# Optimization experiments

Hardware: AMD Instinct MI355X
Metric: run time of the kernel (lower is better)

The kernel has to match this reference:

```python
import jax, jax.numpy as jnp
import numpy as np
import math

# module hyperparams (from init_kwargs)
H = 4          # num_heads
HID = 128      # hid_dim
DK = HID // H  # embed_time_k = 32
DIM = 64       # input_dim (value feature dim)
OUT = 128      # output_dim
NEG = -1e30


def setup_inputs() -> dict:
    key = jax.random.key(0)
    ks = jax.random.split(key, 10)
    B, SQ, SK = 16, 128, 256
    query = jax.random.normal(ks[0], (B, SQ, HID), jnp.float32)
    k_in = jax.random.normal(ks[1], (B, SK, HID), jnp.float32)
    value = jax.random.normal(ks[2], (B, SK, DIM), jnp.float32)
    mask = jax.random.randint(ks[3], (B, SK, DIM), 0, 2).astype(jnp.int32)
    s = 1.0 / math.sqrt(HID)
    Wq = jax.random.uniform(ks[4], (HID, HID), jnp.float32, -s, s)
    bq = jax.random.uniform(ks[5], (HID,), jnp.float32, -s, s)
    Wk = jax.random.uniform(ks[6], (HID, HID), jnp.float32, -s, s)
    bk = jax.random.uniform(ks[7], (HID,), jnp.float32, -s, s)
    so = 1.0 / math.sqrt(DIM * H)
    Wo = jax.random.uniform(ks[8], (OUT, DIM * H), jnp.float32, -so, so)
    bo = jax.random.uniform(ks[9], (OUT,), jnp.float32, -so, so)
    return {"query": query, "key": k_in, "value": value, "mask": mask,
            "Wq": Wq, "bq": bq, "Wk": Wk, "bk": bk, "Wo": Wo, "bo": bo}


def reference(query, key, value, mask, Wq, bq, Wk, bk, Wo, bo):
    B, SQ, _ = query.shape
    _, SK, D = value.shape
    # project and split heads: (B, S, HID) -> (B, H, S, DK)
    q = (query @ Wq.T + bq).reshape(B, SQ, H, DK).transpose(0, 2, 1, 3)
    k = (key @ Wk.T + bk).reshape(B, SK, H, DK).transpose(0, 2, 1, 3)
    # scores: (B, H, SQ, SK)
    scores = jnp.einsum('bhqd,bhkd->bhqk', q, k) / math.sqrt(DK)
    # per-channel mask: scores expand to (B, H, SQ, SK, D)
    m = (mask[:, None, None, :, :] != 0)  # (B,1,1,SK,D)
    scores5 = jnp.where(m, scores[..., None], NEG)
    # softmax over seq_k axis (axis=-2)
    p = jax.nn.softmax(scores5, axis=-2)
    # weighted sum over seq_k: (B, H, SQ, D)
    x = jnp.sum(p * value[:, None, None, :, :], axis=-2)
    # merge heads: (B, SQ, H*D) then output projection
    x = x.transpose(0, 2, 1, 3).reshape(B, SQ, H * D)
    return x @ Wo.T + bo
```

## Files before the change

kernel.cpp:

```cpp
#include <hip/hip_runtime.h>
#include <math.h>

#define B    16
#define SQn  128
#define SEQK 256
#define HID  128
#define NH   4
#define DK   32
#define DIM  64
#define OUTD 128

__global__ __launch_bounds__(256) void transpose3_kernel(
    const float* __restrict__ Wq, const float* __restrict__ Wk,
    const float* __restrict__ Wo,
    float* __restrict__ Wq_t, float* __restrict__ Wk_t, float* __restrict__ Wo_t)
{
    __shared__ float tile[16][17];
    const int z = blockIdx.z;
    const float* src; float* dst; int R, C;
    if (z == 0)      { src = Wq; dst = Wq_t; R = 128; C = 128; }
    else if (z == 1) { src = Wk; dst = Wk_t; R = 128; C = 128; }
    else             { src = Wo; dst = Wo_t; R = 128; C = 256; }
    const int c0 = blockIdx.x * 16, r0 = blockIdx.y * 16;
    if (c0 >= C) return;
    const int tx = threadIdx.x & 15, ty = threadIdx.x >> 4;
    tile[ty][tx] = src[(r0 + ty) * C + (c0 + tx)];
    __syncthreads();
    dst[(c0 + ty) * R + (r0 + tx)] = tile[tx][ty];
}

__global__ __launch_bounds__(256) void prep_kernel(
    const float* __restrict__ value, const int* __restrict__ mask,
    const float* __restrict__ bo, float* __restrict__ MVF, float* __restrict__ out)
{
    const int idx = blockIdx.x * 256 + threadIdx.x;
    const int NMV = B * SEQK * DIM;
    if (idx < NMV) {
        const int d = idx & 63, rest = idx >> 6;
        const float v = value[idx];
        const int   m = mask[idx];
        MVF[rest * 128 + d]      = m ? v : 0.f;
        MVF[rest * 128 + 64 + d] = m ? 1.f : 0.f;
    } else {
        const int o = idx - NMV;
        out[o] = bo[o & 127];
    }
}

__global__ __launch_bounds__(256) void projqk_kernel(
    const float* __restrict__ query, const float* __restrict__ key,
    const float* __restrict__ Wq_t, const float* __restrict__ Wk_t,
    const float* __restrict__ bq, const float* __restrict__ bk,
    float* __restrict__ qp, float* __restrict__ kp_t)
{
    __shared__ float in16[16 * 128];
    const int r0 = blockIdx.x * 16;
    const bool isQ = (r0 < 2048);
    const int t = threadIdx.x;

    const float4* src4 = (const float4*)(isQ ? (query + r0 * 128)
                                             : (key + (r0 - 2048) * 128));
    float4* in4 = (float4*)in16;
    in4[t]       = src4[t];
    in4[t + 256] = src4[t + 256];
    __syncthreads();

    const int j  = t & 127;
    const int rg = (t >> 7) * 8;
    const float* W = isQ ? Wq_t : Wk_t;
    const float bias = isQ ? bq[j] : bk[j];
    float acc[8];
#pragma unroll
    for (int r = 0; r < 8; ++r) acc[r] = bias;

    for (int i4 = 0; i4 < 32; ++i4) {
        const float w0 = W[(i4 * 4 + 0) * 128 + j];
        const float w1 = W[(i4 * 4 + 1) * 128 + j];
        const float w2 = W[(i4 * 4 + 2) * 128 + j];
        const float w3 = W[(i4 * 4 + 3) * 128 + j];
#pragma unroll
        for (int r = 0; r < 8; ++r) {
            float4 xv = ((const float4*)(in16 + (rg + r) * 128))[i4];
            acc[r] = fmaf(xv.x, w0, fmaf(xv.y, w1, fmaf(xv.z, w2, fmaf(xv.w, w3, acc[r]))));
        }
    }

    if (isQ) {
        const float scale = 0.17677669529663687f;
#pragma unroll
        for (int r = 0; r < 8; ++r) qp[(r0 + rg + r) * 128 + j] = acc[r] * scale;
    } else {
#pragma unroll
        for (int r = 0; r < 8; ++r) {
            const int row = r0 - 2048 + rg + r;
            const int bb = row >> 8, k = row & 255;
            kp_t[(bb * 128 + j) * 256 + k] = acc[r];
        }
    }
}

__global__ __launch_bounds__(256) void attn_kernel(
    const float* __restrict__ qp, const float* __restrict__ kp_t,
    const float* __restrict__ MVF, const float* __restrict__ Wo_t,
    float* __restrict__ out)
{
    const int qt = blockIdx.x, h = blockIdx.y, b = blockIdx.z;
    const int q0 = qt * 32;
    const int t  = threadIdx.x;

    __shared__ float qs[32 * 33];
    __shared__ float es[256 * 36];
    __shared__ float red[8 * 33];
    __shared__ float xs[32 * 68];

    {
        const int i = t & 31, qq = t >> 5;
#pragma unroll
        for (int it = 0; it < 4; ++it) {
            const int q = qq + it * 8;
            qs[i * 33 + q] = qp[(b * 128 + q0 + q) * 128 + h * 32 + i];
        }
    }
    __syncthreads();

    const int q = t & 31, kg = t >> 5;
    float s[32];
#pragma unroll
    for (int n = 0; n < 32; ++n) s[n] = 0.f;
    {
        const float4* kpb = (const float4*)(kp_t + (b * 128 + h * 32) * 256) + kg * 8;
        for (int i = 0; i < 32; ++i) {
            const float qv = qs[i * 33 + q];
            const float4* kr = kpb + i * 64;
#pragma unroll
            for (int n = 0; n < 8; ++n) {
                const float4 kv = kr[n];
                s[n * 4 + 0] = fmaf(qv, kv.x, s[n * 4 + 0]);
                s[n * 4 + 1] = fmaf(qv, kv.y, s[n * 4 + 1]);
                s[n * 4 + 2] = fmaf(qv, kv.z, s[n * 4 + 2]);
                s[n * 4 + 3] = fmaf(qv, kv.w, s[n * 4 + 3]);
            }
        }
    }

    {
        float m = s[0];
#pragma unroll
        for (int n = 1; n < 32; ++n) m = fmaxf(m, s[n]);
        red[kg * 33 + q] = m;
    }
    __syncthreads();
    {
        float m = red[q];
#pragma unroll
        for (int rr = 1; rr < 8; ++rr) m = fmaxf(m, red[rr * 33 + q]);
#pragma unroll
        for (int n = 0; n < 32; ++n) es[(kg * 32 + n) * 36 + q] = __expf(s[n] - m);
    }
    __syncthreads();

    const int c = t & 63, qg = t >> 6;
    float num[8], den[8];
#pragma unroll
    for (int i = 0; i < 8; ++i) { num[i] = 0.f; den[i] = 0.f; }
    {
        const float*  mvp = MVF + (b * 256) * 128 + c;
        const float4* e4  = (const float4*)es + qg * 2;
        for (int k = 0; k < 256; ++k) {
            const float4 e0 = e4[k * 9];
            const float4 e1 = e4[k * 9 + 1];
            const float mvv = mvp[k * 128];
            const float mff = mvp[k * 128 + 64];
            num[0] = fmaf(e0.x, mvv, num[0]); den[0] = fmaf(e0.x, mff, den[0]);
            num[1] = fmaf(e0.y, mvv, num[1]); den[1] = fmaf(e0.y, mff, den[1]);
            num[2] = fmaf(e0.z, mvv, num[2]); den[2] = fmaf(e0.z, mff, den[2]);
            num[3] = fmaf(e0.w, mvv, num[3]); den[3] = fmaf(e0.w, mff, den[3]);
            num[4] = fmaf(e1.x, mvv, num[4]); den[4] = fmaf(e1.x, mff, den[4]);
            num[5] = fmaf(e1.y, mvv, num[5]); den[5] = fmaf(e1.y, mff, den[5]);
            num[6] = fmaf(e1.z, mvv, num[6]); den[6] = fmaf(e1.z, mff, den[6]);
            num[7] = fmaf(e1.w, mvv, num[7]); den[7] = fmaf(e1.w, mff, den[7]);
        }
    }
#pragma unroll
    for (int i = 0; i < 8; ++i) xs[(qg * 8 + i) * 68 + c] = num[i] / den[i];
    __syncthreads();

    const int o  = t & 127;
    const int qh = (t >> 7) * 16;
    float acc[16];
#pragma unroll
    for (int i = 0; i < 16; ++i) acc[i] = 0.f;
    {
        const float* wo = Wo_t + (h * 64) * 128 + o;
        for (int j4 = 0; j4 < 16; ++j4) {
            const float w0 = wo[(j4 * 4 + 0) * 128];
            const float w1 = wo[(j4 * 4 + 1) * 128];
            const float w2 = wo[(j4 * 4 + 2) * 128];
            const float w3 = wo[(j4 * 4 + 3) * 128];
#pragma unroll
            for (int i = 0; i < 16; ++i) {
                const float4 xv = ((const float4*)(xs + (qh + i) * 68))[j4];
                acc[i] = fmaf(xv.x, w0, fmaf(xv.y, w1, fmaf(xv.z, w2, fmaf(xv.w, w3, acc[i]))));
            }
        }
    }
#pragma unroll
    for (int i = 0; i < 16; ++i)
        atomicAdd(out + (b * 128 + q0 + qh + i) * 128 + o, acc[i]);
}

extern "C" void kernel_launch(void* const* d_in, const int* in_sizes, int n_in,
                              void* d_out, int out_size, void* d_ws, size_t ws_size,
                              hipStream_t stream)
{
    const float* query = (const float*)d_in[0];
    const float* key   = (const float*)d_in[1];
    const float* value = (const float*)d_in[2];
    const int*   mask  = (const int*)d_in[3];
    const float* Wq    = (const float*)d_in[4];
    const float* bq    = (const float*)d_in[5];
    const float* Wk    = (const float*)d_in[6];
    const float* bk    = (const float*)d_in[7];
    const float* Wo    = (const float*)d_in[8];
    const float* bo    = (const float*)d_in[9];
    float* out = (float*)d_out;

    float* ws   = (float*)d_ws;
    float* Wq_t = ws;
    float* Wk_t = Wq_t + HID * HID;
    float* Wo_t = Wk_t + HID * HID;
    float* qp   = Wo_t + 256 * 128;
    float* kp_t = qp + 2048 * 128;
    float* MVF  = kp_t + 524288;

    transpose3_kernel<<<dim3(16, 8, 3), 256, 0, stream>>>(Wq, Wk, Wo, Wq_t, Wk_t, Wo_t);
    prep_kernel<<<(2 * B * SEQK * DIM) / 256, 256, 0, stream>>>(value, mask, bo, MVF, out);
    projqk_kernel<<<6144 / 16, 256, 0, stream>>>(query, key, Wq_t, Wk_t, bq, bk, qp, kp_t);
    attn_kernel<<<dim3(4, NH, B), 256, 0, stream>>>(qp, kp_t, MVF, Wo_t, out);
}
```

Before: 126.6 us.

## Fuse setup kernels into one launch and halve attention query tile

Merges the weight transpose, mask/value prep and Q/K projection kernels into a single block-indexed setup kernel. The projection now transposes Wq/Wk chunks into shared memory itself, which removes the dependency on a separate transpose pass. Prep is vectorised with float4/int4. The attention kernel uses 16-query tiles instead of 32, doubling the grid to 512 blocks for better occupancy, and the value accumulation is restructured so each thread loads float4 values. The cost is more redundant K loads and more atomics per output.

Result: no change. 128.0 us (+1.1%).

```diff
diff --git a/kernel.cpp b/kernel.cpp
--- a/kernel.cpp
+++ b/kernel.cpp
@@ -2,7 +2,6 @@
 #include <math.h>
 
 #define B    16
-#define SQn  128
 #define SEQK 256
 #define HID  128
 #define NH   4
@@ -10,92 +9,116 @@
 #define DIM  64
 #define OUTD 128
 
-__global__ __launch_bounds__(256) void transpose3_kernel(
-    const float* __restrict__ Wq, const float* __restrict__ Wk,
-    const float* __restrict__ Wo,
-    float* __restrict__ Wq_t, float* __restrict__ Wk_t, float* __restrict__ Wo_t)
+#define NB_PREP 256
+#define NB_PROJ 384
+#define NB_WOT  32
+#define NB_SETUP (NB_PREP + NB_PROJ + NB_WOT)
+
+__global__ __launch_bounds__(256) void setup_kernel(
+    const float* __restrict__ query, const float* __restrict__ key,
+    const float* __restrict__ value, const int* __restrict__ mask,
+    const float* __restrict__ Wq, const float* __restrict__ bq,
+    const float* __restrict__ Wk, const float* __restrict__ bk,
+    const float* __restrict__ Wo, const float* __restrict__ bo,
+    float* __restrict__ qp, float* __restrict__ kp_t,
+    float* __restrict__ MVF, float* __restrict__ Wo_t,
+    float* __restrict__ out)
 {
-    __shared__ float tile[16][17];
-    const int z = blockIdx.z;
-    const float* src; float* dst; int R, C;
-    if (z == 0)      { src = Wq; dst = Wq_t; R = 128; C = 128; }
-    else if (z == 1) { src = Wk; dst = Wk_t; R = 128; C = 128; }
-    else             { src = Wo; dst = Wo_t; R = 128; C = 256; }
-    const int c0 = blockIdx.x * 16, r0 = blockIdx.y * 16;
-    if (c0 >= C) return;
-    const int tx = threadIdx.x & 15, ty = threadIdx.x >> 4;
-    tile[ty][tx] = src[(r0 + ty) * C + (c0 + tx)];
-    __syncthreads();
-    dst[(c0 + ty) * R + (r0 + tx)] = tile[tx][ty];
-}
-
-__global__ __launch_bounds__(256) void prep_kernel(
-    const float* __restrict__ value, const int* __restrict__ mask,
-    const float* __restrict__ bo, float* __restrict__ MVF, float* __restrict__ out)
-{
-    const int idx = blockIdx.x * 256 + threadIdx.x;
-    const int NMV = B * SEQK * DIM;
-    if (idx < NMV) {
-        const int d = idx & 63, rest = idx >> 6;
-        const float v = value[idx];
-        const int   m = mask[idx];
-        MVF[rest * 128 + d]      = m ? v : 0.f;
-        MVF[rest * 128 + 64 + d] = m ? 1.f : 0.f;
+    __shared__ float smem[16 * 128 + 32 * 130];
+    const int bid = blockIdx.x;
+    const int t   = threadIdx.x;
+
+    if (bid < NB_PREP) {
+        const int idx4 = bid * 256 + t;
+        {
+            const float4 v = ((const float4*)value)[idx4];
+            const int4   m = ((const int4*)mask)[idx4];
+            const int d4 = idx4 & 15, row = idx4 >> 4;
+            float4 mv, mf;
+            mv.x = m.x ? v.x : 0.f;  mf.x = m.x ? 1.f : 0.f;
+            mv.y = m.y ? v.y : 0.f;  mf.y = m.y ? 1.f : 0.f;
+            mv.z = m.z ? v.z : 0.f;  mf.z = m.z ? 1.f : 0.f;
+            mv.w = m.w ? v.w : 0.f;  mf.w = m.w ? 1.f : 0.f;
+            ((float4*)(MVF + row * 128))[d4]      = mv;
+            ((float4*)(MVF + row * 128 + 64))[d4] = mf;
+        }
+        {
+            const float4 bv = ((const float4*)bo)[idx4 & 31];
+            ((float4*)out)[idx4] = bv;
+        }
+    } else if (bid < NB_PREP + NB_PROJ) {
+        float* in16 = smem;
+        float* Wt   = smem + 2048;
+        const int r0 = (bid - NB_PREP) * 16;
+        const bool isQ = (r0 < 2048);
+        const float4* src4 = (const float4*)(isQ ? (query + r0 * 128)
+                                                 : (key + (r0 - 2048) * 128));
+        {
+            float4* in4 = (float4*)in16;
+            in4[t]       = src4[t];
+            in4[t + 256] = src4[t + 256];
+        }
+        const float* Wsrc = isQ ? Wq : Wk;
+        const int j  = t & 127;
+        const int rg = (t >> 7) * 8;
+        const float bias = isQ ? bq[j] : bk[j];
+        float acc[8];
+#pragma unroll
+        for (int r = 0; r < 8; ++r) acc[r] = bias;
+
+        for (int ic = 0; ic < 4; ++ic) {
+            __syncthreads();
+            {
+                const int i4 = t & 7, jg = t >> 3;
+#pragma unroll
+                for (int jj = 0; jj < 4; ++jj) {
+                    const int jw = jg + jj * 32;
+                    const float4 w = *(const float4*)(Wsrc + jw * 128 + ic * 32 + i4 * 4);
+                    Wt[(i4 * 4 + 0) * 130 + jw] = w.x;
+                    Wt[(i4 * 4 + 1) * 130 + jw] = w.y;
+                    Wt[(i4 * 4 + 2) * 130 + jw] = w.z;
+                    Wt[(i4 * 4 + 3) * 130 + jw] = w.w;
+                }
+            }
+            __syncthreads();
+#pragma unroll 2
+            for (int i4 = 0; i4 < 8; ++i4) {
+                const float w0 = Wt[(i4 * 4 + 0) * 130 + j];
+                const float w1 = Wt[(i4 * 4 + 1) * 130 + j];
+                const float w2 = Wt[(i4 * 4 + 2) * 130 + j];
+                const float w3 = Wt[(i4 * 4 + 3) * 130 + j];
+#pragma unroll
+                for (int r = 0; r < 8; ++r) {
+                    const float4 xv = ((const float4*)(in16 + (rg + r) * 128))[ic * 8 + i4];
+                    acc[r] = fmaf(xv.x, w0, fmaf(xv.y, w1, fmaf(xv.z, w2, fmaf(xv.w, w3, acc[r]))));
+                }
+            }
+        }
+
+        if (isQ) {
+            const float scale = 0.17677669529663687f;
+#pragma unroll
+            for (int r = 0; r < 8; ++r) qp[(r0 + rg + r) * 128 + j] = acc[r] * scale;
+        } else {
+#pragma unroll
+            for (int r = 0; r < 8; ++r) {
+                const int row = r0 - 2048 + rg + r;
+                const int bb = row >> 8, k = row & 255;
+                kp_t[(bb * 128 + j) * 256 + k] = acc[r];
+            }
+        }
     } else {
-        const int o = idx - NMV;
-        out[o] = bo[o & 127];
-    }
-}
-
-__global__ __launch_bounds__(256) void projqk_kernel(
-    const float* __restrict__ query, const float* __restrict__ key,
-    const float* __restrict__ Wq_t, const float* __restrict__ Wk_t,
-    const float* __restrict__ bq, const float* __restrict__ bk,
-    float* __restrict__ qp, float* __restrict__ kp_t)
-{
-    __shared__ float in16[16 * 128];
-    const int r0 = blockIdx.x * 16;
-    const bool isQ = (r0 < 2048);
-    const int t = threadIdx.x;
-
-    const float4* src4 = (const float4*)(isQ ? (query + r0 * 128)
-                                             : (key + (r0 - 2048) * 128));
-    float4* in4 = (float4*)in16;
-    in4[t]       = src4[t];
-    in4[t + 256] = src4[t + 256];
-    __syncthreads();
-
-    const int j  = t & 127;
-    const int rg = (t >> 7) * 8;
-    const float* W = isQ ? Wq_t : Wk_t;
-    const float bias = isQ ? bq[j] : bk[j];
-    float acc[8];
-#pragma unroll
-    for (int r = 0; r < 8; ++r) acc[r] = bias;
-
-    for (int i4 = 0; i4 < 32; ++i4) {
-        const float w0 = W[(i4 * 4 + 0) * 128 + j];
-        const float w1 = W[(i4 * 4 + 1) * 128 + j];
-        const float w2 = W[(i4 * 4 + 2) * 128 + j];
-        const float w3 = W[(i4 * 4 + 3) * 128 + j];
-#pragma unroll
-        for (int r = 0; r < 8; ++r) {
-            float4 xv = ((const float4*)(in16 + (rg + r) * 128))[i4];
-            acc[r] = fmaf(xv.x, w0, fmaf(xv.y, w1, fmaf(xv.z, w2, fmaf(xv.w, w3, acc[r]))));
-        }
-    }
-
-    if (isQ) {
-        const float scale = 0.17677669529663687f;
-#pragma unroll
-        for (int r = 0; r < 8; ++r) qp[(r0 + rg + r) * 128 + j] = acc[r] * scale;
-    } else {
-#pragma unroll
-        for (int r = 0; r < 8; ++r) {
-            const int row = r0 - 2048 + rg + r;
-            const int bb = row >> 8, k = row & 255;
-            kp_t[(bb * 128 + j) * 256 + k] = acc[r];
-        }
+        float (*tile)[33] = (float (*)[33])smem;
+        const int tt = bid - (NB_PREP + NB_PROJ);
+        const int jt = tt & 7, ot = tt >> 3;
+        const int tx = t & 31, ty = t >> 5;
+#pragma unroll
+        for (int e = 0; e < 4; ++e)
+            tile[ty + e * 8][tx] = Wo[(ot * 32 + ty + e * 8) * 256 + jt * 32 + tx];
+        __syncthreads();
+#pragma unroll
+        for (int e = 0; e < 4; ++e)
+            Wo_t[(jt * 32 + ty + e * 8) * 128 + ot * 32 + tx] = tile[tx][ty + e * 8];
     }
 }
 
@@ -105,35 +128,36 @@
     float* __restrict__ out)
 {
     const int qt = blockIdx.x, h = blockIdx.y, b = blockIdx.z;
-    const int q0 = qt * 32;
+    const int q0 = qt * 16;
     const int t  = threadIdx.x;
 
-    __shared__ float qs[32 * 33];
-    __shared__ float es[256 * 36];
-    __shared__ float red[8 * 33];
-    __shared__ float xs[32 * 68];
+    __shared__ float qs[32 * 17];
+    __shared__ float es[256 * 20];
+    __shared__ float red[16 * 17];
+    __shared__ float xs[16 * 72];
 
     {
         const int i = t & 31, qq = t >> 5;
 #pragma unroll
-        for (int it = 0; it < 4; ++it) {
-            const int q = qq + it * 8;
-            qs[i * 33 + q] = qp[(b * 128 + q0 + q) * 128 + h * 32 + i];
-        }
-    }
-    __syncthreads();
-
-    const int q = t & 31, kg = t >> 5;
-    float s[32];
-#pragma unroll
-    for (int n = 0; n < 32; ++n) s[n] = 0.f;
-    {
-        const float4* kpb = (const float4*)(kp_t + (b * 128 + h * 32) * 256) + kg * 8;
+        for (int e = 0; e < 2; ++e) {
+            const int q = qq + e * 8;
+            qs[i * 17 + q] = qp[(b * 128 + q0 + q) * 128 + h * 32 + i];
+        }
+    }
+    __syncthreads();
+
+    const int q = t & 15, kg = t >> 4;
+    float s[16];
+#pragma unroll
+    for (int n = 0; n < 16; ++n) s[n] = 0.f;
+    {
+        const float4* kpb = (const float4*)(kp_t + (b * 128 + h * 32) * 256) + kg * 4;
+#pragma unroll 4
         for (int i = 0; i < 32; ++i) {
-            const float qv = qs[i * 33 + q];
+            const float qv = qs[i * 17 + q];
             const float4* kr = kpb + i * 64;
 #pragma unroll
-            for (int n = 0; n < 8; ++n) {
+            for (int n = 0; n < 4; ++n) {
                 const float4 kv = kr[n];
                 s[n * 4 + 0] = fmaf(qv, kv.x, s[n * 4 + 0]);
                 s[n * 4 + 1] = fmaf(qv, kv.y, s[n * 4 + 1]);
@@ -146,67 +170,64 @@
     {
         float m = s[0];
 #pragma unroll
-        for (int n = 1; n < 32; ++n) m = fmaxf(m, s[n]);
-        red[kg * 33 + q] = m;
+        for (int n = 1; n < 16; ++n) m = fmaxf(m, s[n]);
+        red[kg * 17 + q] = m;
     }
     __syncthreads();
     {
         float m = red[q];
 #pragma unroll
-        for (int rr = 1; rr < 8; ++rr) m = fmaxf(m, red[rr * 33 + q]);
-#pragma unroll
-        for (int n = 0; n < 32; ++n) es[(kg * 32 + n) * 36 + q] = __expf(s[n] - m);
-    }
-    __syncthreads();
-
-    const int c = t & 63, qg = t >> 6;
-    float num[8], den[8];
-#pragma unroll
-    for (int i = 0; i < 8; ++i) { num[i] = 0.f; den[i] = 0.f; }
-    {
-        const float*  mvp = MVF + (b * 256) * 128 + c;
-        const float4* e4  = (const float4*)es + qg * 2;
+        for (int rr = 1; rr < 16; ++rr) m = fmaxf(m, red[rr * 17 + q]);
+#pragma unroll
+        for (int n = 0; n < 16; ++n) es[(kg * 16 + n) * 20 + q] = __expf(s[n] - m);
+    }
+    __syncthreads();
+
+    {
+        const int c4 = t & 15, qe = t >> 4;
+        const float4* vp = (const float4*)(MVF + b * 256 * 128) + c4;
+        const float4* fp = vp + 16;
+        const float*  ep = es + qe;
+        float n0 = 0.f, n1 = 0.f, n2 = 0.f, n3 = 0.f;
+        float d0 = 0.f, d1 = 0.f, d2 = 0.f, d3 = 0.f;
+#pragma unroll 4
         for (int k = 0; k < 256; ++k) {
-            const float4 e0 = e4[k * 9];
-            const float4 e1 = e4[k * 9 + 1];
-            const float mvv = mvp[k * 128];
-            const float mff = mvp[k * 128 + 64];
-            num[0] = fmaf(e0.x, mvv, num[0]); den[0] = fmaf(e0.x, mff, den[0]);
-            num[1] = fmaf(e0.y, mvv, num[1]); den[1] = fmaf(e0.y, mff, den[1]);
-            num[2] = fmaf(e0.z, mvv, num[2]); den[2] = fmaf(e0.z, mff, den[2]);
-            num[3] = fmaf(e0.w, mvv, num[3]); den[3] = fmaf(e0.w, mff, den[3]);
-            num[4] = fmaf(e1.x, mvv, num[4]); den[4] = fmaf(e1.x, mff, den[4]);
-            num[5] = fmaf(e1.y, mvv, num[5]); den[5] = fmaf(e1.y, mff, den[5]);
-            num[6] = fmaf(e1.z, mvv, num[6]); den[6] = fmaf(e1.z, mff, den[6]);
-            num[7] = fmaf(e1.w, mvv, num[7]); den[7] = fmaf(e1.w, mff, den[7]);
-        }
-    }
-#pragma unroll
-    for (int i = 0; i < 8; ++i) xs[(qg * 8 + i) * 68 + c] = num[i] / den[i];
-    __syncthreads();
-
-    const int o  = t & 127;
-    const int qh = (t >> 7) * 16;
-    float acc[16];
-#pragma unroll
-    for (int i = 0; i < 16; ++i) acc[i] = 0.f;
-    {
+            const float4 v = vp[k * 32];
+            const float4 f = fp[k * 32];
+            const float  e = ep[k * 20];
+            n0 = fmaf(e, v.x, n0); d0 = fmaf(e, f.x, d0);
+            n1 = fmaf(e, v.y, n1); d1 = fmaf(e, f.y, d1);
+            n2 = fmaf(e, v.z, n2); d2 = fmaf(e, f.z, d2);
+            n3 = fmaf(e, v.w, n3); d3 = fmaf(e, f.w, d3);
+        }
+        float4 xv;
+        xv.x = n0 / d0; xv.y = n1 / d1; xv.z = n2 / d2; xv.w = n3 / d3;
+        *(float4*)(xs + qe * 72 + c4 * 4) = xv;
+    }
+    __syncthreads();
+
+    {
+        const int o = t & 127, qh = (t >> 7) * 8;
+        float acc[8];
+#pragma unroll
+        for (int i = 0; i < 8; ++i) acc[i] = 0.f;
         const float* wo = Wo_t + (h * 64) * 128 + o;
+#pragma unroll 2
         for (int j4 = 0; j4 < 16; ++j4) {
             const float w0 = wo[(j4 * 4 + 0) * 128];
             const float w1 = wo[(j4 * 4 + 1) * 128];
             const float w2 = wo[(j4 * 4 + 2) * 128];
             const float w3 = wo[(j4 * 4 + 3) * 128];
 #pragma unroll
-            for (int i = 0; i < 16; ++i) {
-                const float4 xv = ((const float4*)(xs + (qh + i) * 68))[j4];
+            for (int i = 0; i < 8; ++i) {
+                const float4 xv = *(const float4*)(xs + (qh + i) * 72 + j4 * 4);
                 acc[i] = fmaf(xv.x, w0, fmaf(xv.y, w1, fmaf(xv.z, w2, fmaf(xv.w, w3, acc[i]))));
             }
         }
-    }
-#pragma unroll
-    for (int i = 0; i < 16; ++i)
-        atomicAdd(out + (b * 128 + q0 + qh + i) * 128 + o, acc[i]);
+#pragma unroll
+        for (int i = 0; i < 8; ++i)
+            atomicAdd(out + (b * 128 + q0 + qh + i) * 128 + o, acc[i]);
+    }
 }
 
 extern "C" void kernel_launch(void* const* d_in, const int* in_sizes, int n_in,
@@ -226,15 +247,13 @@
     float* out = (float*)d_out;
 
     float* ws   = (float*)d_ws;
-    float* Wq_t = ws;
-    float* Wk_t = Wq_t + HID * HID;
-    float* Wo_t = Wk_t + HID * HID;
+    float* Wo_t = ws;
     float* qp   = Wo_t + 256 * 128;
     float* kp_t = qp + 2048 * 128;
     float* MVF  = kp_t + 524288;
 
-    transpose3_kernel<<<dim3(16, 8, 3), 256, 0, stream>>>(Wq, Wk, Wo, Wq_t, Wk_t, Wo_t);
-    prep_kernel<<<(2 * B * SEQK * DIM) / 256, 256, 0, stream>>>(value, mask, bo, MVF, out);
-    projqk_kernel<<<6144 / 16, 256, 0, stream>>>(query, key, Wq_t, Wk_t, bq, bk, qp, kp_t);
-    attn_kernel<<<dim3(4, NH, B), 256, 0, stream>>>(qp, kp_t, MVF, Wo_t, out);
+    setup_kernel<<<NB_SETUP, 256, 0, stream>>>(query, key, value, mask,
+                                               Wq, bq, Wk, bk, Wo, bo,
+                                               qp, kp_t, MVF, Wo_t, out);
+    attn_kernel<<<dim3(8, NH, B), 256, 0, stream>>>(qp, kp_t, MVF, Wo_t, out);
 }
```
